# Optimization experiments

Measured on AMD Instinct MI355X. Metric: run time of the kernel, lower is better.

The kernel has to match this reference:

```python
import jax, jax.numpy as jnp
import numpy as np

B = 2; GH = 64; GW = 64
D = 384; H = 12; HD = D // H          # head dim 32
SD = 2                                 # spatial dims
KS = 7; ST = 3; PAD = (KS - 1) // 2    # strided conv params
RR = 0.5
NROT = (int(HD * RR) // (2 * SD)) * (2 * SD)   # 16 rotated dims per head
PAIRS = NROT // (2 * SD)                        # 4 freq pairs per spatial axis
ITERS = 3
BASE = 10000.0
LN_EPS = 1e-5
EPS = np.float32(1.1920929e-07)        # torch.finfo(float32).eps


def setup_inputs() -> dict:
    key = jax.random.key(0)
    ks = jax.random.split(key, 8)
    s = 0.02
    # base rotary frequencies with 'sqrt' scaling, per head/axis, + init jitter
    inv = BASE ** (-jnp.arange(PAIRS, dtype=jnp.float32) / PAIRS)
    inv = jnp.sqrt(inv)
    rose_freqs = jnp.broadcast_to(inv, (H, SD, PAIRS)) + 0.02 * jax.random.normal(ks[7], (H, SD, PAIRS), jnp.float32)
    return {
        "x": jax.random.normal(ks[0], (B, GH * GW, D), jnp.float32),
        "conv_w": jax.random.normal(ks[1], (D, D, KS, KS), jnp.float32) / np.float32(np.sqrt(D * KS * KS)),
        "conv_b": jnp.zeros((D,), jnp.float32),
        "kv_w": s * jax.random.normal(ks[2], (D, 2 * D), jnp.float32),
        "kv_b": jnp.zeros((2 * D,), jnp.float32),
        "q_w": s * jax.random.normal(ks[3], (D, D), jnp.float32),
        "q_b": jnp.zeros((D,), jnp.float32),
        "mlp_w1": s * jax.random.normal(ks[4], (D, 4 * D), jnp.float32),
        "mlp_b1": jnp.zeros((4 * D,), jnp.float32),
        "mlp_w2": s * jax.random.normal(ks[5], (4 * D, D), jnp.float32),
        "mlp_b2": jnp.zeros((D,), jnp.float32),
        "g1": jnp.ones((D,), jnp.float32), "b1": jnp.zeros((D,), jnp.float32),
        "g2": jnp.ones((D,), jnp.float32), "b2": jnp.zeros((D,), jnp.float32),
        "g3": jnp.ones((D,), jnp.float32), "b3": jnp.zeros((D,), jnp.float32),
        "temp": jnp.array([1.0 / np.sqrt(D)], jnp.float32),
        "rose_freqs": rose_freqs,
        "grid_h": GH,
        "grid_w": GW,
    }


def _ln(x, g, b):
    mu = jnp.mean(x, axis=-1, keepdims=True)
    var = jnp.mean(jnp.square(x - mu), axis=-1, keepdims=True)
    return (x - mu) * jax.lax.rsqrt(var + LN_EPS) * g + b


def _rose(x, freqs, grid_shape, spacing):
    """Rotary spatial embedding. x: (B, N, D) -> (B, H, N, HD) with first NROT
    head dims rotated by per-head learnable frequencies over real-space coords."""
    Bx, N, _ = x.shape
    axes = [jnp.arange(g, dtype=jnp.float32) * sp for g, sp in zip(grid_shape, spacing)]
    coords = jnp.stack(jnp.meshgrid(*axes, indexing='ij'), axis=-1).reshape(-1, SD)  # (N, SD)
    ang = jnp.einsum('ns,hsp->hnsp', coords, freqs).reshape(H, N, NROT // 2)
    cos = jnp.cos(ang)[None]; sin = jnp.sin(ang)[None]                # (1,H,N,NROT/2)
    xh = x.reshape(Bx, N, H, HD).transpose(0, 2, 1, 3)                # (B,H,N,HD)
    x1 = xh[..., 0:NROT:2]; x2 = xh[..., 1:NROT:2]
    rot = jnp.stack([x1 * cos - x2 * sin, x1 * sin + x2 * cos], axis=-1).reshape(Bx, H, N, NROT)
    return jnp.concatenate([rot, xh[..., NROT:]], axis=-1)


def reference(x, conv_w, conv_b, kv_w, kv_b, q_w, q_b, mlp_w1, mlp_b1, mlp_w2, mlp_b2,
              g1, b1, g2, b2, g3, b3, temp, rose_freqs, grid_h, grid_w):
    in_grid = (int(grid_h), int(grid_w)); in_sp = (1.0, 1.0)
    q_grid = tuple((g + 2 * PAD - KS) // ST + 1 for g in in_grid)
    q_sp = tuple(s * ST for s in in_sp)
    Bx, N_in, _ = x.shape
    N_out = q_grid[0] * q_grid[1]

    # strided conv producing low-res slots, then norm1
    xt = x.transpose(0, 2, 1).reshape(Bx, D, *in_grid)
    xo = jax.lax.conv_general_dilated(xt, conv_w, (ST, ST), [(PAD, PAD), (PAD, PAD)])
    xo = xo + conv_b[None, :, None, None]
    x_out = _ln(xo.reshape(Bx, D, N_out).transpose(0, 2, 1), g1, b1)  # (B,N_out,D)

    attn_q = attn_k = None
    for _ in range(ITERS):
        kv = x @ kv_w + kv_b
        k_lin, v = kv[..., :D], kv[..., D:]
        k = temp * _rose(k_lin, rose_freqs, in_grid, in_sp)           # (B,H,N_in,HD)
        q = _rose(x_out @ q_w + q_b, rose_freqs, q_grid, q_sp)       # (B,H,N_out,HD)
        # concrete attn: softmax over keys of q.k^T (temp already folded into k)
        attn_k = jax.nn.softmax(jnp.einsum('bhqd,bhkd->bhqk', q, k), axis=-1)
        attn_q = attn_k / (jnp.sum(attn_k, axis=-2, keepdims=True) + EPS)
        vh = v.reshape(Bx, N_in, H, HD).transpose(0, 2, 1, 3)
        upd = jnp.einsum('bhqk,bhkd->bhqd', attn_q, vh).transpose(0, 2, 1, 3).reshape(Bx, N_out, D)
        x_out = x_out + _ln(upd, g2, b2)
        h = jax.nn.gelu(x_out @ mlp_w1 + mlp_b1, approximate=False) @ mlp_w2 + mlp_b2
        x_out = x_out + _ln(h, g3, b3)
    return x_out, attn_q, attn_k
```

## Files before the change

kernel.cpp:

```cpp
#include <hip/hip_runtime.h>
#include <math.h>

#define BB 2
#define D_ 384
#define H_ 12
#define HD 32
#define NIN 4096
#define NOUT 484
#define MOUT (BB*NOUT)
#define MIN_ (BB*NIN)
#define QW_ 22
#define CK 18816
#define NSLICE 49
#define LN_EPS 1e-5f
#define EPS_ 1.1920929e-07f

typedef short bf16x8 __attribute__((ext_vector_type(8)));
typedef float f32x4  __attribute__((ext_vector_type(4)));

__device__ __forceinline__ unsigned f2bf(float f){
  unsigned u = __float_as_uint(f);
  u += 0x7fffu + ((u>>16)&1u);
  return u>>16;
}

static const size_t OXOUT = 0;
static const size_t OKB   = 371712;
static const size_t OVH   = OKB + 1572864;
static const size_t OQB   = OVH + 3145728;
static const size_t OQP   = OQB + 196608;
static const size_t OL0   = OQP + 371712;
static const size_t OCS   = OL0 + 12288;
static const size_t OLP   = OCS + 98304;
static const size_t OUPD  = OLP + 196608;
static const size_t OH1   = OUPD + 371712;
static const size_t OH2   = OH1 + 1486848;
static const size_t OQWB  = OH2 + 1486848;
static const size_t OW1B  = OQWB + 73728;
static const size_t OW2B  = OW1B + 294912;

__global__ __launch_bounds__(256)
void packall(const float* __restrict__ px,  ushort* __restrict__ xb,
             const float* __restrict__ cw,  ushort* __restrict__ wtb,
             const float* __restrict__ wkv, ushort* __restrict__ kvwb,
             const float* __restrict__ wq,  ushort* __restrict__ qwb,
             const float* __restrict__ w1,  ushort* __restrict__ w1b,
             const float* __restrict__ w2,  ushort* __restrict__ w2b){
  const int bid = blockIdx.x, t = threadIdx.x;
  if (bid < 3072){
    int base = (bid*256 + t)*4;
    float4 v = *(const float4*)(px + base);
    uint2 o;
    o.x = f2bf(v.x) | (f2bf(v.y)<<16);
    o.y = f2bf(v.z) | (f2bf(v.w)<<16);
    *(uint2*)(xb + base) = o;
  } else if (bid < 31296){
    int i = (bid-3072)*256 + t;
    int n = i / CK;
    int r = i - n*CK;
    int di = r/49, kyx = r - di*49;
    wtb[((size_t)kyx*D_ + n)*D_ + di] = (ushort)f2bf(cw[i]);
  } else if (bid < 32448){
    int i = (bid-31296)*256 + t;
    int k = i/768, n = i - k*768;
    kvwb[(size_t)n*384 + k] = (ushort)f2bf(wkv[i]);
  } else if (bid < 33024){
    int i = (bid-32448)*256 + t;
    int k = i/384, n = i - k*384;
    qwb[(size_t)n*384 + k] = (ushort)f2bf(wq[i]);
  } else if (bid < 35328){
    int i = (bid-33024)*256 + t;
    int k = i/1536, n = i - k*1536;
    w1b[(size_t)n*384 + k] = (ushort)f2bf(w1[i]);
  } else {
    int i = (bid-35328)*256 + t;
    int k = i/384, n = i - k*384;
    w2b[(size_t)n*1536 + k] = (ushort)f2bf(w2[i]);
  }
}

__global__ __launch_bounds__(256)
void convm(const ushort* __restrict__ xb, const ushort* __restrict__ wtb,
           float* __restrict__ part){
  __shared__ ushort As[128][40];
  __shared__ ushort Bs[128][40];
  const int t  = threadIdx.x;
  const int m0 = blockIdx.x*128, n0 = blockIdx.y*128, z = blockIdx.z;
  const int ky = z/7, kx = z - ky*7;
  const int r = t>>1, half = t&1;
  const int m = m0 + r;
  const int mq = (m < MOUT) ? m : 0;
  const int bbv = mq/NOUT, qq = mq - bbv*NOUT;
  const int oy = qq/QW_, ox = qq - oy*QW_;
  const int iy = oy*3-3+ky, ix = ox*3-3+kx;
  const bool aval = (m<MOUT) && iy>=0 && iy<64 && ix>=0 && ix<64;
  const ushort* asrc = xb + ((size_t)bbv*NIN + (aval ? iy*64+ix : 0))*D_ + half*16;
  const ushort* bsrc = wtb + ((size_t)z*D_ + n0 + r)*D_ + half*16;

  const int wv = t>>6;
  const int wr = (wv>>1)*64, wc = (wv&1)*64;
  const int ln = t&15, lq = (t>>4)&3;

  f32x4 acc[4][4];
#pragma unroll
  for (int i=0;i<4;i++)
#pragma unroll
    for (int j=0;j<4;j++) acc[i][j] = (f32x4){0.f,0.f,0.f,0.f};

  for (int dk=0; dk<D_; dk+=32){
    uint4 a0 = {0,0,0,0}, a1 = {0,0,0,0};
    if (aval){ a0 = *(const uint4*)(asrc+dk); a1 = *(const uint4*)(asrc+dk+8); }
    uint4 b0 = *(const uint4*)(bsrc+dk), b1 = *(const uint4*)(bsrc+dk+8);
    *(uint4*)&As[r][half*16]   = a0;  *(uint4*)&As[r][half*16+8] = a1;
    *(uint4*)&Bs[r][half*16]   = b0;  *(uint4*)&Bs[r][half*16+8] = b1;
    __syncthreads();
    bf16x8 af[4], bfr[4];
#pragma unroll
    for (int i=0;i<4;i++) af[i]  = *(const bf16x8*)&As[wr+i*16+ln][lq*8];
#pragma unroll
    for (int j=0;j<4;j++) bfr[j] = *(const bf16x8*)&Bs[wc+j*16+ln][lq*8];
#pragma unroll
    for (int i=0;i<4;i++)
#pragma unroll
      for (int j=0;j<4;j++)
        acc[i][j] = __builtin_amdgcn_mfma_f32_16x16x32_bf16(af[i], bfr[j], acc[i][j], 0,0,0);
    __syncthreads();
  }
#pragma unroll
  for (int i=0;i<4;i++){
    int rowb = m0 + wr + i*16 + lq*4;
#pragma unroll
    for (int j=0;j<4;j++){
      int col = n0 + wc + j*16 + ln;
#pragma unroll
      for (int rg=0; rg<4; rg++){
        int row = rowb + rg;
        if (row < MOUT) part[((size_t)z*MOUT + row)*D_ + col] = acc[i][j][rg];
      }
    }
  }
}

template<int ACT, bool ABF>
__global__ __launch_bounds__(256)
void gemmm(const void* __restrict__ Ain, const ushort* __restrict__ Wb,
           const float* __restrict__ bias, float* __restrict__ C,
           int M, int N, int K){
  __shared__ ushort As[128][40];
  __shared__ ushort Bs[128][40];
  const int t  = threadIdx.x;
  const int m0 = blockIdx.x*128, n0 = blockIdx.y*128;
  const int r = t>>1, half = t&1;
  const int m = m0 + r;
  const bool aval = (m < M);
  const float*  af32 = (const float*)Ain  + (size_t)(aval?m:0)*K + half*16;
  const ushort* ab16 = (const ushort*)Ain + (size_t)(aval?m:0)*K + half*16;
  const ushort* bsrc = Wb + (size_t)(n0 + r)*K + half*16;

  const int wv = t>>6;
  const int wr = (wv>>1)*64, wc = (wv&1)*64;
  const int ln = t&15, lq = (t>>4)&3;

  f32x4 acc[4][4];
#pragma unroll
  for (int i=0;i<4;i++)
#pragma unroll
    for (int j=0;j<4;j++) acc[i][j] = (f32x4){0.f,0.f,0.f,0.f};

  for (int dk=0; dk<K; dk+=32){
    uint4 a0 = {0,0,0,0}, a1 = {0,0,0,0};
    if (aval){
      if (ABF){
        a0 = *(const uint4*)(ab16+dk); a1 = *(const uint4*)(ab16+dk+8);
      } else {
        float4 f0 = *(const float4*)(af32+dk),   f1 = *(const float4*)(af32+dk+4);
        float4 f2 = *(const float4*)(af32+dk+8), f3 = *(const float4*)(af32+dk+12);
        a0.x = f2bf(f0.x)|(f2bf(f0.y)<<16); a0.y = f2bf(f0.z)|(f2bf(f0.w)<<16);
        a0.z = f2bf(f1.x)|(f2bf(f1.y)<<16); a0.w = f2bf(f1.z)|(f2bf(f1.w)<<16);
        a1.x = f2bf(f2.x)|(f2bf(f2.y)<<16); a1.y = f2bf(f2.z)|(f2bf(f2.w)<<16);
        a1.z = f2bf(f3.x)|(f2bf(f3.y)<<16); a1.w = f2bf(f3.z)|(f2bf(f3.w)<<16);
      }
    }
    uint4 b0 = *(const uint4*)(bsrc+dk), b1 = *(const uint4*)(bsrc+dk+8);
    *(uint4*)&As[r][half*16]   = a0;  *(uint4*)&As[r][half*16+8] = a1;
    *(uint4*)&Bs[r][half*16]   = b0;  *(uint4*)&Bs[r][half*16+8] = b1;
    __syncthreads();
    bf16x8 af[4], bfr[4];
#pragma unroll
    for (int i=0;i<4;i++) af[i]  = *(const bf16x8*)&As[wr+i*16+ln][lq*8];
#pragma unroll
    for (int j=0;j<4;j++) bfr[j] = *(const bf16x8*)&Bs[wc+j*16+ln][lq*8];
#pragma unroll
    for (int i=0;i<4;i++)
#pragma unroll
      for (int j=0;j<4;j++)
        acc[i][j] = __builtin_amdgcn_mfma_f32_16x16x32_bf16(af[i], bfr[j], acc[i][j], 0,0,0);
    __syncthreads();
  }
#pragma unroll
  for (int i=0;i<4;i++){
    int rowb = m0 + wr + i*16 + lq*4;
#pragma unroll
    for (int j=0;j<4;j++){
      int col = n0 + wc + j*16 + ln;
      float bv = bias[col];
#pragma unroll
      for (int rg=0; rg<4; rg++){
        int row = rowb + rg;
        if (row < M){
          float v = acc[i][j][rg] + bv;
          if (ACT==1) v = 0.5f*v*(1.f + erff(v*0.7071067811865475f));
          C[(size_t)row*N + col] = v;
        }
      }
    }
  }
}

template<int ACT>
__global__ __launch_bounds__(256)
void gemm64(const float* __restrict__ Ain, const ushort* __restrict__ Wb,
            const float* __restrict__ bias, float* __restrict__ C,
            int M, int N, int K){
  __shared__ ushort As[64][40];
  __shared__ ushort Bs[64][40];
  const int t  = threadIdx.x;
  const int m0 = blockIdx.x*64, n0 = blockIdx.y*64;
  const int r = t>>2, seg = t&3;
  const int m = m0 + r;
  const bool aval = (m < M);
  const float*  asrc = Ain + (size_t)(aval?m:0)*K + seg*8;
  const ushort* bsrc = Wb + (size_t)(n0 + r)*K + seg*8;

  const int wv = t>>6;
  const int wr = (wv>>1)*32, wc = (wv&1)*32;
  const int ln = t&15, lq = (t>>4)&3;

  f32x4 acc[2][2];
  acc[0][0]=(f32x4){0,0,0,0}; acc[0][1]=(f32x4){0,0,0,0};
  acc[1][0]=(f32x4){0,0,0,0}; acc[1][1]=(f32x4){0,0,0,0};

  for (int dk=0; dk<K; dk+=32){
    uint4 a0 = {0,0,0,0};
    if (aval){
      float4 f0 = *(const float4*)(asrc+dk), f1 = *(const float4*)(asrc+dk+4);
      a0.x = f2bf(f0.x)|(f2bf(f0.y)<<16); a0.y = f2bf(f0.z)|(f2bf(f0.w)<<16);
      a0.z = f2bf(f1.x)|(f2bf(f1.y)<<16); a0.w = f2bf(f1.z)|(f2bf(f1.w)<<16);
    }
    uint4 b0 = *(const uint4*)(bsrc+dk);
    *(uint4*)&As[r][seg*8] = a0;
    *(uint4*)&Bs[r][seg*8] = b0;
    __syncthreads();
    bf16x8 af[2], bfr[2];
#pragma unroll
    for (int i=0;i<2;i++) af[i]  = *(const bf16x8*)&As[wr+i*16+ln][lq*8];
#pragma unroll
    for (int j=0;j<2;j++) bfr[j] = *(const bf16x8*)&Bs[wc+j*16+ln][lq*8];
#pragma unroll
    for (int i=0;i<2;i++)
#pragma unroll
      for (int j=0;j<2;j++)
        acc[i][j] = __builtin_amdgcn_mfma_f32_16x16x32_bf16(af[i], bfr[j], acc[i][j], 0,0,0);
    __syncthreads();
  }
#pragma unroll
  for (int i=0;i<2;i++){
    int rowb = m0 + wr + i*16 + lq*4;
#pragma unroll
    for (int j=0;j<2;j++){
      int col = n0 + wc + j*16 + ln;
      float bv = bias[col];
#pragma unroll
      for (int rg=0; rg<4; rg++){
        int row = rowb + rg;
        if (row < M){
          float v = acc[i][j][rg] + bv;
          if (ACT==1) v = 0.5f*v*(1.f + erff(v*0.7071067811865475f));
          C[(size_t)row*N + col] = v;
        }
      }
    }
  }
}

__global__ __launch_bounds__(256)
void gemm64sk(const float* __restrict__ Ain, const ushort* __restrict__ Wb,
              float* __restrict__ part){
  __shared__ ushort As[64][40];
  __shared__ ushort Bs[64][40];
  const int t  = threadIdx.x;
  const int m0 = blockIdx.x*64, n0 = blockIdx.y*64, z = blockIdx.z;
  const int r = t>>2, seg = t&3;
  const int m = m0 + r;
  const bool aval = (m < MOUT);
  const float*  asrc = Ain + (size_t)(aval?m:0)*1536 + z*384 + seg*8;
  const ushort* bsrc = Wb + (size_t)(n0 + r)*1536 + z*384 + seg*8;

  const int wv = t>>6;
  const int wr = (wv>>1)*32, wc = (wv&1)*32;
  const int ln = t&15, lq = (t>>4)&3;

  f32x4 acc[2][2];
  acc[0][0]=(f32x4){0,0,0,0}; acc[0][1]=(f32x4){0,0,0,0};
  acc[1][0]=(f32x4){0,0,0,0}; acc[1][1]=(f32x4){0,0,0,0};

  for (int dk=0; dk<384; dk+=32){
    uint4 a0 = {0,0,0,0};
    if (aval){
      float4 f0 = *(const float4*)(asrc+dk), f1 = *(const float4*)(asrc+dk+4);
      a0.x = f2bf(f0.x)|(f2bf(f0.y)<<16); a0.y = f2bf(f0.z)|(f2bf(f0.w)<<16);
      a0.z = f2bf(f1.x)|(f2bf(f1.y)<<16); a0.w = f2bf(f1.z)|(f2bf(f1.w)<<16);
    }
    uint4 b0 = *(const uint4*)(bsrc+dk);
    *(uint4*)&As[r][seg*8] = a0;
    *(uint4*)&Bs[r][seg*8] = b0;
    __syncthreads();
    bf16x8 af[2], bfr[2];
#pragma unroll
    for (int i=0;i<2;i++) af[i]  = *(const bf16x8*)&As[wr+i*16+ln][lq*8];
#pragma unroll
    for (int j=0;j<2;j++) bfr[j] = *(const bf16x8*)&Bs[wc+j*16+ln][lq*8];
#pragma unroll
    for (int i=0;i<2;i++)
#pragma unroll
      for (int j=0;j<2;j++)
        acc[i][j] = __builtin_amdgcn_mfma_f32_16x16x32_bf16(af[i], bfr[j], acc[i][j], 0,0,0);
    __syncthreads();
  }
#pragma unroll
  for (int i=0;i<2;i++){
    int rowb = m0 + wr + i*16 + lq*4;
#pragma unroll
    for (int j=0;j<2;j++){
      int col = n0 + wc + j*16 + ln;
#pragma unroll
      for (int rg=0; rg<4; rg++){
        int row = rowb + rg;
        if (row < MOUT) part[((size_t)z*MOUT + row)*D_ + col] = acc[i][j][rg];
      }
    }
  }
}

__device__ __forceinline__ float block_sum_384(float v){
  __shared__ float red[6];
#pragma unroll
  for (int o=32;o>0;o>>=1) v += __shfl_down(v,o);
  const int lane = threadIdx.x & 63, w = threadIdx.x >> 6;
  __syncthreads();
  if (lane==0) red[w] = v;
  __syncthreads();
  return red[0]+red[1]+red[2]+red[3]+red[4]+red[5];
}

template<int MODE>
__global__ __launch_bounds__(384)
void lnk(const float* __restrict__ in, const float* __restrict__ cb,
         const float* __restrict__ gg, const float* __restrict__ bb,
         float* __restrict__ xout){
  const int m = blockIdx.x, d = threadIdx.x;
  float v;
  if (MODE==0){
    v = cb[d];
    for (int z=0; z<NSLICE; z++) v += in[((size_t)z*MOUT + m)*D_ + d];
  } else if (MODE==1){
    int b = m/NOUT, q = m - b*NOUT;
    int h = d>>5, dd2 = d&31;
    v = in[(((size_t)(b*H_ + h))*NOUT + q)*HD + dd2];
  } else {
    v = cb[d];
#pragma unroll
    for (int z=0; z<4; z++) v += in[((size_t)z*MOUT + m)*D_ + d];
  }
  float mu  = block_sum_384(v) * (1.f/D_);
  float ce  = v - mu;
  float var = block_sum_384(ce*ce) * (1.f/D_);
  float o = ce * rsqrtf(var + LN_EPS) * gg[d] + bb[d];
  float* dst = xout + (size_t)m*D_ + d;
  if (MODE==0) *dst = o;
  else *dst += o;
}

__global__ __launch_bounds__(256)
void rosek(const float* __restrict__ kvbuf, const float* __restrict__ rf,
           const float* __restrict__ temp,
           ushort* __restrict__ kb, float* __restrict__ vhb){
  int idx = blockIdx.x*256 + threadIdx.x;
  if (idx >= BB*H_*NIN) return;
  int n  = idx & (NIN-1);
  int bh = idx >> 12;
  int h  = bh % H_;
  int b  = bh / H_;
  float T = temp[0];
  int iy = n >> 6, ix = n & 63;
  const float* src = kvbuf + ((size_t)b*NIN + n)*768 + h*HD;
  float xv[HD];
#pragma unroll
  for (int d4=0; d4<8; d4++){
    float4 v = *(const float4*)(src + d4*4);
    xv[d4*4]=v.x; xv[d4*4+1]=v.y; xv[d4*4+2]=v.z; xv[d4*4+3]=v.w;
  }
  float out[HD];
#pragma unroll
  for (int tp=0; tp<8; tp++){
    int s2 = tp >> 2, p2 = tp & 3;
    float coord = (s2==0) ? (float)iy : (float)ix;
    float ang = coord * rf[(h*2+s2)*4 + p2];
    float sn, cn; sincosf(ang, &sn, &cn);
    float x1 = xv[2*tp], x2 = xv[2*tp+1];
    out[2*tp]   = x1*cn - x2*sn;
    out[2*tp+1] = x1*sn + x2*cn;
  }
#pragma unroll
  for (int d=16; d<HD; d++) out[d] = xv[d];
  ushort* dk = kb + ((size_t)bh*NIN + n)*HD;
#pragma unroll
  for (int g=0; g<4; g++){
    uint4 o;
    o.x = f2bf(T*out[g*8+0]) | (f2bf(T*out[g*8+1])<<16);
    o.y = f2bf(T*out[g*8+2]) | (f2bf(T*out[g*8+3])<<16);
    o.z = f2bf(T*out[g*8+4]) | (f2bf(T*out[g*8+5])<<16);
    o.w = f2bf(T*out[g*8+6]) | (f2bf(T*out[g*8+7])<<16);
    *(uint4*)(dk + g*8) = o;
  }
  const float* vs = src + D_;
  float* dv = vhb + ((size_t)bh*NIN + n)*HD;
#pragma unroll
  for (int d4=0; d4<8; d4++)
    *(float4*)(dv + d4*4) = *(const float4*)(vs + d4*4);
}

__global__ __launch_bounds__(256)
void roseq(const float* __restrict__ qp, const float* __restrict__ rf,
           ushort* __restrict__ qb){
  int idx = blockIdx.x*256 + threadIdx.x;
  int q  = idx & 511;
  int bh = idx >> 9;
  int h  = bh % H_;
  int b  = bh / H_;
  ushort* dq = qb + ((size_t)bh*512 + q)*HD;
  if (q >= NOUT){
    uint4 z = {0,0,0,0};
#pragma unroll
    for (int g=0; g<4; g++) *(uint4*)(dq + g*8) = z;
    return;
  }
  int oy = q / QW_, ox = q - oy*QW_;
  const float* src = qp + ((size_t)b*NOUT + q)*D_ + h*HD;
  float xv[HD];
#pragma unroll
  for (int d4=0; d4<8; d4++){
    float4 v = *(const float4*)(src + d4*4);
    xv[d4*4]=v.x; xv[d4*4+1]=v.y; xv[d4*4+2]=v.z; xv[d4*4+3]=v.w;
  }
  float out[HD];
#pragma unroll
  for (int tp=0; tp<8; tp++){
    int s2 = tp >> 2, p2 = tp & 3;
    float coord = (s2==0) ? 3.0f*(float)oy : 3.0f*(float)ox;
    float ang = coord * rf[(h*2+s2)*4 + p2];
    float sn, cn; sincosf(ang, &sn, &cn);
    float x1 = xv[2*tp], x2 = xv[2*tp+1];
    out[2*tp]   = x1*cn - x2*sn;
    out[2*tp+1] = x1*sn + x2*cn;
  }
#pragma unroll
  for (int d=16; d<HD; d++) out[d] = xv[d];
#pragma unroll
  for (int g=0; g<4; g++){
    uint4 o;
    o.x = f2bf(out[g*8+0]) | (f2bf(out[g*8+1])<<16);
    o.y = f2bf(out[g*8+2]) | (f2bf(out[g*8+3])<<16);
    o.z = f2bf(out[g*8+4]) | (f2bf(out[g*8+5])<<16);
    o.w = f2bf(out[g*8+6]) | (f2bf(out[g*8+7])<<16);
    *(uint4*)(dq + g*8) = o;
  }
}

__global__ __launch_bounds__(256)
void rowk(const ushort* __restrict__ qb, const ushort* __restrict__ kb,
          float* __restrict__ l0part){
  __shared__ ushort Qs[64][40];
  __shared__ ushort Ks[256][40];
  __shared__ float  red[4][64];
  const int t  = threadIdx.x;
  const int q0 = blockIdx.x*64;
  const int kt = blockIdx.y;
  const int k0 = kt*256;
  const int bh = blockIdx.z;
  {
    int row = t>>2, seg = t&3;
    const ushort* src = qb + ((size_t)bh*512 + q0 + row)*HD + seg*8;
    *(uint4*)&Qs[row][seg*8] = *(const uint4*)src;
  }
  {
    const ushort* src = kb + ((size_t)bh*NIN + k0 + t)*HD;
#pragma unroll
    for (int g=0; g<4; g++)
      *(uint4*)&Ks[t][g*8] = *(const uint4*)(src + g*8);
  }
  __syncthreads();
  const int wv = t>>6;
  const int wc = wv*64;
  const int ln = t&15, lq = (t>>4)&3;
  bf16x8 af[4], bfr[4];
#pragma unroll
  for (int i=0;i<4;i++) af[i]  = *(const bf16x8*)&Qs[i*16+ln][lq*8];
#pragma unroll
  for (int j=0;j<4;j++) bfr[j] = *(const bf16x8*)&Ks[wc+j*16+ln][lq*8];
  f32x4 acc[4][4];
  const f32x4 zero = (f32x4){0.f,0.f,0.f,0.f};
#pragma unroll
  for (int i=0;i<4;i++)
#pragma unroll
    for (int j=0;j<4;j++)
      acc[i][j] = __builtin_amdgcn_mfma_f32_16x16x32_bf16(af[i], bfr[j], zero, 0,0,0);
  float rs[4][4];
#pragma unroll
  for (int i=0;i<4;i++){
#pragma unroll
    for (int rg=0; rg<4; rg++){
      float s = 0.f;
#pragma unroll
      for (int j=0;j<4;j++) s += __expf(acc[i][j][rg]);
      rs[i][rg] = s;
    }
  }
#pragma unroll
  for (int i=0;i<4;i++)
#pragma unroll
    for (int rg=0;rg<4;rg++){
      float v = rs[i][rg];
      v += __shfl_xor(v,1); v += __shfl_xor(v,2);
      v += __shfl_xor(v,4); v += __shfl_xor(v,8);
      rs[i][rg] = v;
    }
  if (ln==0){
#pragma unroll
    for (int i=0;i<4;i++)
#pragma unroll
      for (int rg=0;rg<4;rg++)
        red[wv][i*16+lq*4+rg] = rs[i][rg];
  }
  __syncthreads();
  if (t < 64){
    float tot = red[0][t]+red[1][t]+red[2][t]+red[3][t];
    l0part[((size_t)bh*512 + q0 + t)*16 + kt] = tot;
  }
}

__global__ __launch_bounds__(256)
void colk_f(const ushort* __restrict__ qb, const ushort* __restrict__ kb,
            const float* __restrict__ l0part, float* __restrict__ csinv){
  __shared__ ushort Ks[256][40];
  __shared__ ushort Qs[64][40];
  __shared__ float  lis[64];
  const int t  = threadIdx.x;
  const int k0 = blockIdx.x*256;
  const int bh = blockIdx.y;
  {
    const ushort* src = kb + ((size_t)bh*NIN + k0 + t)*HD;
#pragma unroll
    for (int g=0; g<4; g++)
      *(uint4*)&Ks[t][g*8] = *(const uint4*)(src + g*8);
  }
  const int wv = t>>6, ln = t&15, lq = (t>>4)&3;
  const f32x4 zero = (f32x4){0.f,0.f,0.f,0.f};
  f32x4 colacc[4];
#pragma unroll
  for (int i=0;i<4;i++) colacc[i] = zero;
  for (int qc=0; qc<512; qc+=64){
    __syncthreads();
    {
      int row = t>>2, seg = t&3;
      *(uint4*)&Qs[row][seg*8] =
        *(const uint4*)(qb + ((size_t)bh*512 + qc + row)*HD + seg*8);
    }
    if (t < 64){
      int q = qc + t;
      const float* lp = l0part + ((size_t)bh*512 + q)*16;
      float s = 0.f;
#pragma unroll
      for (int j=0;j<16;j++) s += lp[j];
      lis[t] = (q < NOUT) ? 1.f/s : 0.f;
    }
    __syncthreads();
    bf16x8 af[4], bfr[4];
#pragma unroll
    for (int i=0;i<4;i++) af[i]  = *(const bf16x8*)&Ks[wv*64+i*16+ln][lq*8];
#pragma unroll
    for (int j=0;j<4;j++) bfr[j] = *(const bf16x8*)&Qs[j*16+ln][lq*8];
#pragma unroll
    for (int j=0;j<4;j++){
      float liv = lis[j*16+ln];
#pragma unroll
      for (int i=0;i<4;i++){
        f32x4 c = __builtin_amdgcn_mfma_f32_16x16x32_bf16(af[i], bfr[j], zero, 0,0,0);
#pragma unroll
        for (int rg=0;rg<4;rg++)
          colacc[i][rg] += __expf(c[rg]) * liv;
      }
    }
  }
#pragma unroll
  for (int i=0;i<4;i++)
#pragma unroll
    for (int rg=0;rg<4;rg++){
      float v = colacc[i][rg];
      v += __shfl_xor(v,1); v += __shfl_xor(v,2);
      v += __shfl_xor(v,4); v += __shfl_xor(v,8);
      colacc[i][rg] = v;
    }
  if (ln==0){
#pragma unroll
    for (int i=0;i<4;i++){
      float4 o;
      o.x = 1.f/(colacc[i][0] + EPS_);
      o.y = 1.f/(colacc[i][1] + EPS_);
      o.z = 1.f/(colacc[i][2] + EPS_);
      o.w = 1.f/(colacc[i][3] + EPS_);
      *(float4*)(csinv + (size_t)bh*NIN + k0 + wv*64 + i*16 + lq*4) = o;
    }
  }
}

template<bool LAST>
__global__ __launch_bounds__(256)
void pv_f(const ushort* __restrict__ qb, const ushort* __restrict__ kb,
          const float* __restrict__ vh, const float* __restrict__ l0part,
          const float* __restrict__ csinv, float* __restrict__ upd,
          float* __restrict__ attnq, float* __restrict__ attnk){
  __shared__ ushort   Qs[32][40];
  __shared__ float    Ps[128][36];
  __shared__ unsigned Vt[32][132];
  __shared__ float    lis[32];
  __shared__ float    cis[128];
  const int t  = threadIdx.x;
  const int q0 = blockIdx.x*32;
  const int bh = blockIdx.y;
  {
    int row = t>>3, seg = t&7;
    *(uint2*)&Qs[row][seg*4] =
      *(const uint2*)(qb + ((size_t)bh*512 + q0 + row)*HD + seg*4);
  }
  if (t < 32){
    int q = q0 + t;
    const float* lp = l0part + ((size_t)bh*512 + q)*16;
    float s = 0.f;
#pragma unroll
    for (int j=0;j<16;j++) s += lp[j];
    lis[t] = (q < NOUT) ? 1.f/s : 0.f;
  }
  __syncthreads();
  const int wv = t>>6, ln = t&15, lq = (t>>4)&3;
  const bf16x8 af0 = *(const bf16x8*)&Qs[ln][lq*8];
  const bf16x8 af1 = *(const bf16x8*)&Qs[16+ln][lq*8];
  float lr[2][4];
#pragma unroll
  for (int i=0;i<2;i++)
#pragma unroll
    for (int rg=0;rg<4;rg++) lr[i][rg] = lis[i*16 + lq*4 + rg];
  const f32x4 zero = (f32x4){0.f,0.f,0.f,0.f};
  f32x4 acc[2][2];
  acc[0][0]=zero; acc[0][1]=zero; acc[1][0]=zero; acc[1][1]=zero;
  const ushort* kfrag = kb + ((size_t)bh*NIN)*HD;
  for (int kc=0; kc<NIN; kc+=128){
    if (LAST) __syncthreads();
    {
      int r = t>>1, half = t&1;
      float civ = csinv[(size_t)bh*NIN + kc + r];
      if (half==0) cis[r] = civ;
      const float* pv = vh + ((size_t)bh*NIN + kc + r)*HD + half*16;
      float4 b0=*(const float4*)pv, b1=*(const float4*)(pv+4),
             b2=*(const float4*)(pv+8), b3=*(const float4*)(pv+12);
      float w[16] = {civ*b0.x, civ*b0.y, civ*b0.z, civ*b0.w,
                     civ*b1.x, civ*b1.y, civ*b1.z, civ*b1.w,
                     civ*b2.x, civ*b2.y, civ*b2.z, civ*b2.w,
                     civ*b3.x, civ*b3.y, civ*b3.z, civ*b3.w};
      int dbase = half*16;
#pragma unroll
      for (int i2=0;i2<16;i2++){
        unsigned hi = f2bf(w[i2]);
        float hif = __uint_as_float(hi<<16);
        unsigned lo = f2bf(w[i2] - hif);
        Vt[dbase+i2][r] = (hi<<16) | lo;
      }
    }
    bf16x8 bf0 = *(const bf16x8*)(kfrag + (size_t)(kc + wv*32 +      ln)*HD + lq*8);
    bf16x8 bf1 = *(const bf16x8*)(kfrag + (size_t)(kc + wv*32 + 16 + ln)*HD + lq*8);
    {
      f32x4 c; float4 pw;
      c = __builtin_amdgcn_mfma_f32_16x16x32_bf16(af0, bf0, zero, 0,0,0);
      pw.x=__expf(c[0])*lr[0][0]; pw.y=__expf(c[1])*lr[0][1];
      pw.z=__expf(c[2])*lr[0][2]; pw.w=__expf(c[3])*lr[0][3];
      *(float4*)&Ps[wv*32 +      ln][      lq*4] = pw;
      c = __builtin_amdgcn_mfma_f32_16x16x32_bf16(af1, bf0, zero, 0,0,0);
      pw.x=__expf(c[0])*lr[1][0]; pw.y=__expf(c[1])*lr[1][1];
      pw.z=__expf(c[2])*lr[1][2]; pw.w=__expf(c[3])*lr[1][3];
      *(float4*)&Ps[wv*32 +      ln][16 + lq*4] = pw;
      c = __builtin_amdgcn_mfma_f32_16x16x32_bf16(af0, bf1, zero, 0,0,0);
      pw.x=__expf(c[0])*lr[0][0]; pw.y=__expf(c[1])*lr[0][1];
      pw.z=__expf(c[2])*lr[0][2]; pw.w=__expf(c[3])*lr[0][3];
      *(float4*)&Ps[wv*32 + 16 + ln][      lq*4] = pw;
      c = __builtin_amdgcn_mfma_f32_16x16x32_bf16(af1, bf1, zero, 0,0,0);
      pw.x=__expf(c[0])*lr[1][0]; pw.y=__expf(c[1])*lr[1][1];
      pw.z=__expf(c[2])*lr[1][2]; pw.w=__expf(c[3])*lr[1][3];
      *(float4*)&Ps[wv*32 + 16 + ln][16 + lq*4] = pw;
    }
    if (LAST){
      __syncthreads();
      int row = t>>3, seg = t&7;
      int q = q0 + row;
      if (q < NOUT){
        float* ak = attnk + ((size_t)bh*NOUT + q)*NIN + kc + seg*16;
        float* aq = attnq + ((size_t)bh*NOUT + q)*NIN + kc + seg*16;
#pragma unroll
        for (int s=0;s<4;s++){
          int kk = seg*16 + s*4;
          float4 p = make_float4(Ps[kk][row], Ps[kk+1][row], Ps[kk+2][row], Ps[kk+3][row]);
          float4 c4 = *(const float4*)&cis[kk];
          *(float4*)(ak + s*4) = p;
          float4 pq;
          pq.x = p.x*c4.x; pq.y = p.y*c4.y; pq.z = p.z*c4.z; pq.w = p.w*c4.w;
          *(float4*)(aq + s*4) = pq;
        }
      }
    }
    bf16x8 bhi[2], blo[2];
#pragma unroll
    for (int nf=0;nf<2;nf++){
#pragma unroll
      for (int j=0;j<8;j++){
        float p = Ps[wv*32 + lq*8 + j][nf*16 + ln];
        unsigned hi = f2bf(p);
        float hif = __uint_as_float(hi<<16);
        unsigned lo = f2bf(p - hif);
        bhi[nf][j] = (short)hi;
        blo[nf][j] = (short)lo;
      }
    }
    bf16x8 ahi[2], alo[2];
#pragma unroll
    for (int mf=0;mf<2;mf++){
      const unsigned* vrow = &Vt[mf*16+ln][wv*32 + lq*8];
      uint4 wa = *(const uint4*)vrow;
      uint4 wb = *(const uint4*)(vrow+4);
      ahi[mf][0]=(short)(wa.x>>16); alo[mf][0]=(short)(wa.x&0xffffu);
      ahi[mf][1]=(short)(wa.y>>16); alo[mf][1]=(short)(wa.y&0xffffu);
      ahi[mf][2]=(short)(wa.z>>16); alo[mf][2]=(short)(wa.z&0xffffu);
      ahi[mf][3]=(short)(wa.w>>16); alo[mf][3]=(short)(wa.w&0xffffu);
      ahi[mf][4]=(short)(wb.x>>16); alo[mf][4]=(short)(wb.x&0xffffu);
      ahi[mf][5]=(short)(wb.y>>16); alo[mf][5]=(short)(wb.y&0xffffu);
      ahi[mf][6]=(short)(wb.z>>16); alo[mf][6]=(short)(wb.z&0xffffu);
      ahi[mf][7]=(short)(wb.w>>16); alo[mf][7]=(short)(wb.w&0xffffu);
    }
#pragma unroll
    for (int mf=0;mf<2;mf++)
#pragma unroll
      for (int nf=0;nf<2;nf++){
        acc[mf][nf] = __builtin_amdgcn_mfma_f32_16x16x32_bf16(ahi[mf], bhi[nf], acc[mf][nf], 0,0,0);
        acc[mf][nf] = __builtin_amdgcn_mfma_f32_16x16x32_bf16(ahi[mf], blo[nf], acc[mf][nf], 0,0,0);
        acc[mf][nf] = __builtin_amdgcn_mfma_f32_16x16x32_bf16(alo[mf], bhi[nf], acc[mf][nf], 0,0,0);
      }
  }
  __syncthreads();
  float* Ured = &Ps[0][0];
  {
    int lane = t & 63;
#pragma unroll
    for (int mf=0;mf<2;mf++)
#pragma unroll
      for (int nf=0;nf<2;nf++)
#pragma unroll
        for (int rg=0;rg<4;rg++)
          Ured[wv*1024 + (mf*2+nf)*256 + rg*64 + lane] = acc[mf][nf][rg];
  }
  __syncthreads();
#pragma unroll
  for (int i=0;i<4;i++){
    int s = i*256 + t;
    float u = Ured[s] + Ured[1024+s] + Ured[2048+s] + Ured[3072+s];
    int grp = s>>8, rg = (s>>6)&3, lane = s&63;
    int mf = grp>>1, nf = grp&1;
    int q = q0 + nf*16 + (lane&15);
    int d = mf*16 + (lane>>4)*4 + rg;
    if (q < NOUT) upd[((size_t)bh*NOUT + q)*HD + d] = u;
  }
}

__global__ __launch_bounds__(256)
void copyk(const float* __restrict__ src, float* __restrict__ dst, int n){
  int i = blockIdx.x*256 + threadIdx.x;
  if (i < n) dst[i] = src[i];
}

extern "C" void kernel_launch(void* const* d_in, const int* in_sizes, int n_in,
                              void* d_out, int out_size, void* d_ws, size_t ws_size,
                              hipStream_t stream){
  (void)in_sizes; (void)n_in; (void)out_size; (void)ws_size;
  const float* px    = (const float*)d_in[0];
  const float* pcw   = (const float*)d_in[1];
  const float* pcb   = (const float*)d_in[2];
  const float* pkvw  = (const float*)d_in[3];
  const float* pkvb  = (const float*)d_in[4];
  const float* pqw   = (const float*)d_in[5];
  const float* pqb   = (const float*)d_in[6];
  const float* pw1   = (const float*)d_in[7];
  const float* pb1   = (const float*)d_in[8];
  const float* pw2   = (const float*)d_in[9];
  const float* pb2   = (const float*)d_in[10];
  const float* pg1   = (const float*)d_in[11];
  const float* pbe1  = (const float*)d_in[12];
  const float* pg2   = (const float*)d_in[13];
  const float* pbe2  = (const float*)d_in[14];
  const float* pg3   = (const float*)d_in[15];
  const float* pbe3  = (const float*)d_in[16];
  const float* ptemp = (const float*)d_in[17];
  const float* prf   = (const float*)d_in[18];

  float* out = (float*)d_out;
  float* ws  = (float*)d_ws;

  float* xout   = ws + OXOUT;
  ushort* kb    = (ushort*)(ws + OKB);
  float* vhb    = ws + OVH;
  ushort* qb    = (ushort*)(ws + OQB);
  float* qp     = ws + OQP;
  float* csinv  = ws + OCS;
  float* l0part = ws + OLP;
  float* updb   = ws + OUPD;
  float* h1     = ws + OH1;
  float* h2p    = ws + OH2;
  ushort* qwb   = (ushort*)(ws + OQWB);
  ushort* w1b   = (ushort*)(ws + OW1B);
  ushort* w2b   = (ushort*)(ws + OW2B);

  float* attnq = out + 371712;
  float* attnk = out + 371712 + 47579136;
  float* kvbuf = attnq;
  float* cpart = attnq + 8388608;
  ushort* wtb  = (ushort*)attnk;
  ushort* xb16 = (ushort*)(attnk + 3612672);
  ushort* kvwb = (ushort*)(attnk + 3612672 + 1572864);

  packall<<<dim3(37632), 256, 0, stream>>>(px, xb16, pcw, wtb, pkvw, kvwb,
                                           pqw, qwb, pw1, w1b, pw2, w2b);

  convm<<<dim3(8,3,NSLICE), 256, 0, stream>>>(xb16, wtb, cpart);
  lnk<0><<<dim3(MOUT), 384, 0, stream>>>(cpart, pcb, pg1, pbe1, xout);
  gemmm<0,true><<<dim3(64,6), 256, 0, stream>>>(xb16, kvwb, pkvb, kvbuf, MIN_, 768, 384);
  rosek<<<dim3((BB*H_*NIN+255)/256), 256, 0, stream>>>(kvbuf, prf, ptemp, kb, vhb);

  for (int it=0; it<3; ++it){
    gemm64<0><<<dim3(16,6), 256, 0, stream>>>(xout, qwb, pqb, qp, MOUT, 384, 384);
    roseq<<<dim3(48), 256, 0, stream>>>(qp, prf, qb);
    rowk<<<dim3(8,16,24), 256, 0, stream>>>(qb, kb, l0part);
    colk_f<<<dim3(16,24), 256, 0, stream>>>(qb, kb, l0part, csinv);
    if (it==2){
      pv_f<true ><<<dim3(16,24), 256, 0, stream>>>(qb, kb, vhb, l0part, csinv, updb, attnq, attnk);
    } else {
      pv_f<false><<<dim3(16,24), 256, 0, stream>>>(qb, kb, vhb, l0part, csinv, updb, attnq, attnk);
    }
    lnk<1><<<dim3(MOUT), 384, 0, stream>>>(updb, pcb, pg2, pbe2, xout);
    gemm64<1><<<dim3(16,24), 256, 0, stream>>>(xout, w1b, pb1, h1, MOUT, 1536, 384);
    gemm64sk<<<dim3(16,6,4), 256, 0, stream>>>(h1, w2b, h2p);
    lnk<3><<<dim3(MOUT), 384, 0, stream>>>(h2p, pb2, pg3, pbe3, xout);
  }

  copyk<<<dim3((371712+255)/256), 256, 0, stream>>>(xout, out, 371712);
}
```

Measured before the change: 1.067 ms.

## Fuse RoSE rotation into K/V and Q GEMM epilogues, drop copy kernel

Folds the rotary spatial embedding and bf16 packing of K (with temperature) and V reshaping into the KV projection GEMM epilogue, using a lane shuffle to fetch the rotation partner. The Q projection gets the same treatment, and the zero padding of the Q rows is moved into the one-time pack kernel. The final LayerNorm writes straight to the output, so the trailing copy kernel goes away. This removes fp32 intermediate round trips and several launches, at the cost of scattered 2-byte stores and sincos work inside the GEMM epilogues.

```diff
diff --git a/kernel.cpp b/kernel.cpp
--- a/kernel.cpp
+++ b/kernel.cpp
@@ -45,7 +45,8 @@
              const float* __restrict__ wkv, ushort* __restrict__ kvwb,
              const float* __restrict__ wq,  ushort* __restrict__ qwb,
              const float* __restrict__ w1,  ushort* __restrict__ w1b,
-             const float* __restrict__ w2,  ushort* __restrict__ w2b){
+             const float* __restrict__ w2,  ushort* __restrict__ w2b,
+             ushort* __restrict__ qbpad){
   const int bid = blockIdx.x, t = threadIdx.x;
   if (bid < 3072){
     int base = (bid*256 + t)*4;
@@ -72,10 +73,17 @@
     int i = (bid-33024)*256 + t;
     int k = i/1536, n = i - k*1536;
     w1b[(size_t)n*384 + k] = (ushort)f2bf(w1[i]);
-  } else {
+  } else if (bid < 37632){
     int i = (bid-35328)*256 + t;
     int k = i/384, n = i - k*384;
     w2b[(size_t)n*1536 + k] = (ushort)f2bf(w2[i]);
+  } else {
+    int idx = (bid-37632)*256 + t;
+    int e  = idx*2;
+    int bh = e / 896;
+    int rm = e - bh*896;
+    int rr = rm >> 5, d = rm & 31;
+    *(unsigned*)(qbpad + ((size_t)bh*512 + 484 + rr)*HD + d) = 0u;
   }
 }
 
@@ -141,21 +149,19 @@
   }
 }
 
-template<int ACT, bool ABF>
 __global__ __launch_bounds__(256)
-void gemmm(const void* __restrict__ Ain, const ushort* __restrict__ Wb,
-           const float* __restrict__ bias, float* __restrict__ C,
-           int M, int N, int K){
+void gemmkv(const ushort* __restrict__ Ain, const ushort* __restrict__ Wb,
+            const float* __restrict__ bias, const float* __restrict__ rf,
+            const float* __restrict__ temp,
+            ushort* __restrict__ kb, float* __restrict__ vhb){
   __shared__ ushort As[128][40];
   __shared__ ushort Bs[128][40];
   const int t  = threadIdx.x;
   const int m0 = blockIdx.x*128, n0 = blockIdx.y*128;
   const int r = t>>1, half = t&1;
   const int m = m0 + r;
-  const bool aval = (m < M);
-  const float*  af32 = (const float*)Ain  + (size_t)(aval?m:0)*K + half*16;
-  const ushort* ab16 = (const ushort*)Ain + (size_t)(aval?m:0)*K + half*16;
-  const ushort* bsrc = Wb + (size_t)(n0 + r)*K + half*16;
+  const ushort* ab16 = Ain + (size_t)m*384 + half*16;
+  const ushort* bsrc = Wb + (size_t)(n0 + r)*384 + half*16;
 
   const int wv = t>>6;
   const int wr = (wv>>1)*64, wc = (wv&1)*64;
@@ -167,20 +173,8 @@
 #pragma unroll
     for (int j=0;j<4;j++) acc[i][j] = (f32x4){0.f,0.f,0.f,0.f};
 
-  for (int dk=0; dk<K; dk+=32){
-    uint4 a0 = {0,0,0,0}, a1 = {0,0,0,0};
-    if (aval){
-      if (ABF){
-        a0 = *(const uint4*)(ab16+dk); a1 = *(const uint4*)(ab16+dk+8);
-      } else {
-        float4 f0 = *(const float4*)(af32+dk),   f1 = *(const float4*)(af32+dk+4);
-        float4 f2 = *(const float4*)(af32+dk+8), f3 = *(const float4*)(af32+dk+12);
-        a0.x = f2bf(f0.x)|(f2bf(f0.y)<<16); a0.y = f2bf(f0.z)|(f2bf(f0.w)<<16);
-        a0.z = f2bf(f1.x)|(f2bf(f1.y)<<16); a0.w = f2bf(f1.z)|(f2bf(f1.w)<<16);
-        a1.x = f2bf(f2.x)|(f2bf(f2.y)<<16); a1.y = f2bf(f2.z)|(f2bf(f2.w)<<16);
-        a1.z = f2bf(f3.x)|(f2bf(f3.y)<<16); a1.w = f2bf(f3.z)|(f2bf(f3.w)<<16);
-      }
-    }
+  for (int dk=0; dk<384; dk+=32){
+    uint4 a0 = *(const uint4*)(ab16+dk), a1 = *(const uint4*)(ab16+dk+8);
     uint4 b0 = *(const uint4*)(bsrc+dk), b1 = *(const uint4*)(bsrc+dk+8);
     *(uint4*)&As[r][half*16]   = a0;  *(uint4*)&As[r][half*16+8] = a1;
     *(uint4*)&Bs[r][half*16]   = b0;  *(uint4*)&Bs[r][half*16+8] = b1;
@@ -197,6 +191,7 @@
         acc[i][j] = __builtin_amdgcn_mfma_f32_16x16x32_bf16(af[i], bfr[j], acc[i][j], 0,0,0);
     __syncthreads();
   }
+  const float T = temp[0];
 #pragma unroll
   for (int i=0;i<4;i++){
     int rowb = m0 + wr + i*16 + lq*4;
@@ -207,10 +202,102 @@
 #pragma unroll
       for (int rg=0; rg<4; rg++){
         int row = rowb + rg;
-        if (row < M){
-          float v = acc[i][j][rg] + bv;
-          if (ACT==1) v = 0.5f*v*(1.f + erff(v*0.7071067811865475f));
-          C[(size_t)row*N + col] = v;
+        float v = acc[i][j][rg] + bv;
+        float partner = __shfl_xor(v, 1);
+        int b = row >> 12, n = row & 4095;
+        int iy = n >> 6, ix = n & 63;
+        if (col < 384){
+          int h = col >> 5, d = col & 31;
+          float res = v;
+          if (d < 16){
+            int tp = d >> 1, s2 = tp >> 2, p2 = tp & 3;
+            float coord = (s2==0) ? (float)iy : (float)ix;
+            float ang = coord * rf[(h*2+s2)*4 + p2];
+            float sn, cn; sincosf(ang, &sn, &cn);
+            res = (d & 1) ? (partner*sn + v*cn) : (v*cn - partner*sn);
+          }
+          kb[((size_t)(b*H_ + h)*NIN + n)*HD + d] = (ushort)f2bf(T*res);
+        } else {
+          int c2 = col - 384;
+          int h = c2 >> 5, d = c2 & 31;
+          vhb[((size_t)(b*H_ + h)*NIN + n)*HD + d] = v;
+        }
+      }
+    }
+  }
+}
+
+__global__ __launch_bounds__(256)
+void gemm64q(const float* __restrict__ Ain, const ushort* __restrict__ Wb,
+             const float* __restrict__ bias, const float* __restrict__ rf,
+             ushort* __restrict__ qb){
+  __shared__ ushort As[64][40];
+  __shared__ ushort Bs[64][40];
+  const int t  = threadIdx.x;
+  const int m0 = blockIdx.x*64, n0 = blockIdx.y*64;
+  const int r = t>>2, seg = t&3;
+  const int m = m0 + r;
+  const bool aval = (m < MOUT);
+  const float*  asrc = Ain + (size_t)(aval?m:0)*384 + seg*8;
+  const ushort* bsrc = Wb + (size_t)(n0 + r)*384 + seg*8;
+
+  const int wv = t>>6;
+  const int wr = (wv>>1)*32, wc = (wv&1)*32;
+  const int ln = t&15, lq = (t>>4)&3;
+
+  f32x4 acc[2][2];
+  acc[0][0]=(f32x4){0,0,0,0}; acc[0][1]=(f32x4){0,0,0,0};
+  acc[1][0]=(f32x4){0,0,0,0}; acc[1][1]=(f32x4){0,0,0,0};
+
+  for (int dk=0; dk<384; dk+=32){
+    uint4 a0 = {0,0,0,0};
+    if (aval){
+      float4 f0 = *(const float4*)(asrc+dk), f1 = *(const float4*)(asrc+dk+4);
+      a0.x = f2bf(f0.x)|(f2bf(f0.y)<<16); a0.y = f2bf(f0.z)|(f2bf(f0.w)<<16);
+      a0.z = f2bf(f1.x)|(f2bf(f1.y)<<16); a0.w = f2bf(f1.z)|(f2bf(f1.w)<<16);
+    }
+    uint4 b0 = *(const uint4*)(bsrc+dk);
+    *(uint4*)&As[r][seg*8] = a0;
+    *(uint4*)&Bs[r][seg*8] = b0;
+    __syncthreads();
+    bf16x8 af[2], bfr[2];
+#pragma unroll
+    for (int i=0;i<2;i++) af[i]  = *(const bf16x8*)&As[wr+i*16+ln][lq*8];
+#pragma unroll
+    for (int j=0;j<2;j++) bfr[j] = *(const bf16x8*)&Bs[wc+j*16+ln][lq*8];
+#pragma unroll
+    for (int i=0;i<2;i++)
+#pragma unroll
+      for (int j=0;j<2;j++)
+        acc[i][j] = __builtin_amdgcn_mfma_f32_16x16x32_bf16(af[i], bfr[j], acc[i][j], 0,0,0);
+    __syncthreads();
+  }
+#pragma unroll
+  for (int i=0;i<2;i++){
+    int rowb = m0 + wr + i*16 + lq*4;
+#pragma unroll
+    for (int j=0;j<2;j++){
+      int col = n0 + wc + j*16 + ln;
+      float bv = bias[col];
+#pragma unroll
+      for (int rg=0; rg<4; rg++){
+        int row = rowb + rg;
+        float v = acc[i][j][rg] + bv;
+        float partner = __shfl_xor(v, 1);
+        if (row < MOUT){
+          int b = (row >= NOUT) ? 1 : 0;
+          int q = row - b*NOUT;
+          int oy = q / QW_, ox = q - oy*QW_;
+          int h = col >> 5, d = col & 31;
+          float res = v;
+          if (d < 16){
+            int tp = d >> 1, s2 = tp >> 2, p2 = tp & 3;
+            float coord = (s2==0) ? 3.0f*(float)oy : 3.0f*(float)ox;
+            float ang = coord * rf[(h*2+s2)*4 + p2];
+            float sn, cn; sincosf(ang, &sn, &cn);
+            res = (d & 1) ? (partner*sn + v*cn) : (v*cn - partner*sn);
+          }
+          qb[((size_t)(b*H_ + h)*512 + q)*HD + d] = (ushort)f2bf(res);
         }
       }
     }
@@ -353,11 +440,11 @@
   return red[0]+red[1]+red[2]+red[3]+red[4]+red[5];
 }
 
-template<int MODE>
+template<int MODE, bool FINAL>
 __global__ __launch_bounds__(384)
 void lnk(const float* __restrict__ in, const float* __restrict__ cb,
          const float* __restrict__ gg, const float* __restrict__ bb,
-         float* __restrict__ xout){
+         float* __restrict__ xout, float* __restrict__ fout){
   const int m = blockIdx.x, d = threadIdx.x;
   float v;
   if (MODE==0){
@@ -377,104 +464,9 @@
   float var = block_sum_384(ce*ce) * (1.f/D_);
   float o = ce * rsqrtf(var + LN_EPS) * gg[d] + bb[d];
   float* dst = xout + (size_t)m*D_ + d;
-  if (MODE==0) *dst = o;
-  else *dst += o;
-}
-
-__global__ __launch_bounds__(256)
-void rosek(const float* __restrict__ kvbuf, const float* __restrict__ rf,
-           const float* __restrict__ temp,
-           ushort* __restrict__ kb, float* __restrict__ vhb){
-  int idx = blockIdx.x*256 + threadIdx.x;
-  if (idx >= BB*H_*NIN) return;
-  int n  = idx & (NIN-1);
-  int bh = idx >> 12;
-  int h  = bh % H_;
-  int b  = bh / H_;
-  float T = temp[0];
-  int iy = n >> 6, ix = n & 63;
-  const float* src = kvbuf + ((size_t)b*NIN + n)*768 + h*HD;
-  float xv[HD];
-#pragma unroll
-  for (int d4=0; d4<8; d4++){
-    float4 v = *(const float4*)(src + d4*4);
-    xv[d4*4]=v.x; xv[d4*4+1]=v.y; xv[d4*4+2]=v.z; xv[d4*4+3]=v.w;
-  }
-  float out[HD];
-#pragma unroll
-  for (int tp=0; tp<8; tp++){
-    int s2 = tp >> 2, p2 = tp & 3;
-    float coord = (s2==0) ? (float)iy : (float)ix;
-    float ang = coord * rf[(h*2+s2)*4 + p2];
-    float sn, cn; sincosf(ang, &sn, &cn);
-    float x1 = xv[2*tp], x2 = xv[2*tp+1];
-    out[2*tp]   = x1*cn - x2*sn;
-    out[2*tp+1] = x1*sn + x2*cn;
-  }
-#pragma unroll
-  for (int d=16; d<HD; d++) out[d] = xv[d];
-  ushort* dk = kb + ((size_t)bh*NIN + n)*HD;
-#pragma unroll
-  for (int g=0; g<4; g++){
-    uint4 o;
-    o.x = f2bf(T*out[g*8+0]) | (f2bf(T*out[g*8+1])<<16);
-    o.y = f2bf(T*out[g*8+2]) | (f2bf(T*out[g*8+3])<<16);
-    o.z = f2bf(T*out[g*8+4]) | (f2bf(T*out[g*8+5])<<16);
-    o.w = f2bf(T*out[g*8+6]) | (f2bf(T*out[g*8+7])<<16);
-    *(uint4*)(dk + g*8) = o;
-  }
-  const float* vs = src + D_;
-  float* dv = vhb + ((size_t)bh*NIN + n)*HD;
-#pragma unroll
-  for (int d4=0; d4<8; d4++)
-    *(float4*)(dv + d4*4) = *(const float4*)(vs + d4*4);
-}
-
-__global__ __launch_bounds__(256)
-void roseq(const float* __restrict__ qp, const float* __restrict__ rf,
-           ushort* __restrict__ qb){
-  int idx = blockIdx.x*256 + threadIdx.x;
-  int q  = idx & 511;
-  int bh = idx >> 9;
-  int h  = bh % H_;
-  int b  = bh / H_;
-  ushort* dq = qb + ((size_t)bh*512 + q)*HD;
-  if (q >= NOUT){
-    uint4 z = {0,0,0,0};
-#pragma unroll
-    for (int g=0; g<4; g++) *(uint4*)(dq + g*8) = z;
-    return;
-  }
-  int oy = q / QW_, ox = q - oy*QW_;
-  const float* src = qp + ((size_t)b*NOUT + q)*D_ + h*HD;
-  float xv[HD];
-#pragma unroll
-  for (int d4=0; d4<8; d4++){
-    float4 v = *(const float4*)(src + d4*4);
-    xv[d4*4]=v.x; xv[d4*4+1]=v.y; xv[d4*4+2]=v.z; xv[d4*4+3]=v.w;
-  }
-  float out[HD];
-#pragma unroll
-  for (int tp=0; tp<8; tp++){
-    int s2 = tp >> 2, p2 = tp & 3;
-    float coord = (s2==0) ? 3.0f*(float)oy : 3.0f*(float)ox;
-    float ang = coord * rf[(h*2+s2)*4 + p2];
-    float sn, cn; sincosf(ang, &sn, &cn);
-    float x1 = xv[2*tp], x2 = xv[2*tp+1];
-    out[2*tp]   = x1*cn - x2*sn;
-    out[2*tp+1] = x1*sn + x2*cn;
-  }
-#pragma unroll
-  for (int d=16; d<HD; d++) out[d] = xv[d];
-#pragma unroll
-  for (int g=0; g<4; g++){
-    uint4 o;
-    o.x = f2bf(out[g*8+0]) | (f2bf(out[g*8+1])<<16);
-    o.y = f2bf(out[g*8+2]) | (f2bf(out[g*8+3])<<16);
-    o.z = f2bf(out[g*8+4]) | (f2bf(out[g*8+5])<<16);
-    o.w = f2bf(out[g*8+6]) | (f2bf(out[g*8+7])<<16);
-    *(uint4*)(dq + g*8) = o;
-  }
+  if (MODE==0)       *dst = o;
+  else if (FINAL)    fout[(size_t)m*D_ + d] = *dst + o;
+  else               *dst += o;
 }
 
 __global__ __launch_bounds__(256)
@@ -786,12 +778,6 @@
     int d = mf*16 + (lane>>4)*4 + rg;
     if (q < NOUT) upd[((size_t)bh*NOUT + q)*HD + d] = u;
   }
-}
-
-__global__ __launch_bounds__(256)
-void copyk(const float* __restrict__ src, float* __restrict__ dst, int n){
-  int i = blockIdx.x*256 + threadIdx.x;
-  if (i < n) dst[i] = src[i];
 }
 
 extern "C" void kernel_launch(void* const* d_in, const int* in_sizes, int n_in,
@@ -825,7 +811,6 @@
   ushort* kb    = (ushort*)(ws + OKB);
   float* vhb    = ws + OVH;
   ushort* qb    = (ushort*)(ws + OQB);
-  float* qp     = ws + OQP;
   float* csinv  = ws + OCS;
   float* l0part = ws + OLP;
   float* updb   = ws + OUPD;
@@ -837,23 +822,20 @@
 
   float* attnq = out + 371712;
   float* attnk = out + 371712 + 47579136;
-  float* kvbuf = attnq;
   float* cpart = attnq + 8388608;
   ushort* wtb  = (ushort*)attnk;
   ushort* xb16 = (ushort*)(attnk + 3612672);
   ushort* kvwb = (ushort*)(attnk + 3612672 + 1572864);
 
-  packall<<<dim3(37632), 256, 0, stream>>>(px, xb16, pcw, wtb, pkvw, kvwb,
-                                           pqw, qwb, pw1, w1b, pw2, w2b);
+  packall<<<dim3(37674), 256, 0, stream>>>(px, xb16, pcw, wtb, pkvw, kvwb,
+                                           pqw, qwb, pw1, w1b, pw2, w2b, qb);
 
   convm<<<dim3(8,3,NSLICE), 256, 0, stream>>>(xb16, wtb, cpart);
-  lnk<0><<<dim3(MOUT), 384, 0, stream>>>(cpart, pcb, pg1, pbe1, xout);
-  gemmm<0,true><<<dim3(64,6), 256, 0, stream>>>(xb16, kvwb, pkvb, kvbuf, MIN_, 768, 384);
-  rosek<<<dim3((BB*H_*NIN+255)/256), 256, 0, stream>>>(kvbuf, prf, ptemp, kb, vhb);
+  lnk<0,false><<<dim3(MOUT), 384, 0, stream>>>(cpart, pcb, pg1, pbe1, xout, nullptr);
+  gemmkv<<<dim3(64,6), 256, 0, stream>>>(xb16, kvwb, pkvb, prf, ptemp, kb, vhb);
 
   for (int it=0; it<3; ++it){
-    gemm64<0><<<dim3(16,6), 256, 0, stream>>>(xout, qwb, pqb, qp, MOUT, 384, 384);
-    roseq<<<dim3(48), 256, 0, stream>>>(qp, prf, qb);
+    gemm64q<<<dim3(16,6), 256, 0, stream>>>(xout, qwb, pqb, prf, qb);
     rowk<<<dim3(8,16,24), 256, 0, stream>>>(qb, kb, l0part);
     colk_f<<<dim3(16,24), 256, 0, stream>>>(qb, kb, l0part, csinv);
     if (it==2){
@@ -861,11 +843,13 @@
     } else {
       pv_f<false><<<dim3(16,24), 256, 0, stream>>>(qb, kb, vhb, l0part, csinv, updb, attnq, attnk);
     }
-    lnk<1><<<dim3(MOUT), 384, 0, stream>>>(updb, pcb, pg2, pbe2, xout);
+    lnk<1,false><<<dim3(MOUT), 384, 0, stream>>>(updb, pcb, pg2, pbe2, xout, nullptr);
     gemm64<1><<<dim3(16,24), 256, 0, stream>>>(xout, w1b, pb1, h1, MOUT, 1536, 384);
     gemm64sk<<<dim3(16,6,4), 256, 0, stream>>>(h1, w2b, h2p);
-    lnk<3><<<dim3(MOUT), 384, 0, stream>>>(h2p, pb2, pg3, pbe3, xout);
-  }
-
-  copyk<<<dim3((371712+255)/256), 256, 0, stream>>>(xout, out, 371712);
-}
+    if (it==2){
+      lnk<3,true ><<<dim3(MOUT), 384, 0, stream>>>(h2p, pb2, pg3, pbe3, xout, out);
+    } else {
+      lnk<3,false><<<dim3(MOUT), 384, 0, stream>>>(h2p, pb2, pg3, pbe3, xout, nullptr);
+    }
+  }
+}
```

New measurement: 1.054 ms. About the same (-1.3%).
